# Optimization experiments

Measured on AMD Instinct MI355X. Metric: run time of the kernel, lower is better.

## Reference

```python
import jax, jax.numpy as jnp
import numpy as np

N, D, C = 4096, 2048, 128
MARGIN = 0.3


def _choice(key, mask):
    # Uniform random choice among True entries of mask (Gumbel-max trick).
    g = jax.random.gumbel(key, mask.shape, jnp.float32)
    return jnp.argmax(jnp.where(mask, g, -jnp.inf))


def setup_inputs() -> dict:
    key = jax.random.key(0)
    k1, k2, k3, k4, k5 = jax.random.split(key, 5)
    return {
        "inputs": jax.random.normal(k1, (N, D), jnp.float32),
        "prediction": jax.random.normal(k2, (N, C), jnp.float32),
        "targets": jax.random.randint(k3, (N,), 0, C),
        "true_targets": jax.random.randint(k4, (N,), 0, C),
        "prob": jax.random.uniform(k5, (N,), jnp.float32),
        "threshold": jnp.float32(0.5),
    }


def _forward(inputs, prediction, prob, threshold, targets, true_targets):
    n = inputs.shape[0]
    # Pairwise Euclidean distances: ||xi||^2 + ||xj||^2 - 2 xi.xj  (clamped, sqrt)
    sq = jnp.sum(inputs * inputs, axis=1)
    dist = jnp.sqrt(jnp.clip(sq[:, None] + sq[None, :] - 2.0 * (inputs @ inputs.T), 1e-12, None))
    is_pos = targets[:, None] == targets[None, :]
    confident = prob >= threshold
    pred_cls = jnp.argmax(prediction, axis=1)

    # 12 closest negatives per row (rank 0 = hardest; ranks 1..11 cover the
    # original's fallback loop of at most 10 extra steps, j in 1..11).
    neg_dist = jnp.where(is_pos, jnp.inf, dist)
    _, neg_rank = jax.lax.top_k(-neg_dist, 12)  # [n, 12] indices

    row_keys = jax.random.split(jax.random.key(42), n)
    idx = jnp.arange(n)

    def per_row(i, rk):
        di = dist[i]
        pos_mask = is_pos[i]
        kp, kr = jax.random.split(rk)
        rp = _choice(kp, pos_mask & (idx != i))  # random positive != anchor
        hn = neg_rank[i, 0]                      # hardest negative
        ap0, an0 = di[rp], di[hn]
        p_pos = prob[rp] >= threshold
        p_neg = prob[hn] >= threshold
        is_FN = pred_cls[hn] == targets[i]

        # Case B (pos confident, neg unconfident, false-negative):
        # first confident negative among ranks 1..11, else rank 11.
        cand = neg_rank[i, 1:12]
        conf_c = prob[cand] >= threshold
        hn_new = cand[jnp.where(jnp.any(conf_c), jnp.argmax(conf_c), 10)]
        apB, anB = (ap0 + an0) * 0.5, di[hn_new]

        # Cases C / D-not-FN: resample positive, up to 6 draws total,
        # first draw that is confident and != anchor, else the last draw.
        draws = jax.vmap(lambda k: _choice(k, pos_mask))(jax.random.split(kr, 6))
        valid = (draws != i) & (prob[draws] >= threshold)
        rp_new = draws[jnp.where(jnp.any(valid), jnp.argmax(valid), 5)]
        apC, anC = di[rp_new], (ap0 + an0) * 0.5

        useB = p_pos & ~p_neg & is_FN
        useC = (~p_pos & p_neg) | (~p_pos & ~p_neg & ~is_FN)
        inverse = ~p_pos & ~p_neg & is_FN  # keep ap0/an0, flip hinge direction

        ap = jnp.where(useB, apB, jnp.where(useC, apC, ap0))
        an = jnp.where(useB, anB, jnp.where(useC, anC, an0))
        per_loss = jnp.where(inverse,
                             jnp.maximum(an - ap + MARGIN, 0.0),
                             jnp.maximum(ap - an + MARGIN, 0.0))
        return ap, an, per_loss

    aps, ans, losses = jax.vmap(per_row)(idx, row_keys)
    cnt = jnp.sum(confident)
    loss_sum = jnp.sum(jnp.where(confident, losses, 0.0))
    loss = jnp.where(cnt > 0, loss_sum / jnp.maximum(cnt, 1).astype(loss_sum.dtype),
                     jnp.zeros((), loss_sum.dtype))
    correct = jnp.sum(confident & (ans >= aps))
    return loss, correct, cnt


def reference(inputs, prediction, targets, true_targets, prob, threshold):
    return _forward(inputs, prediction, prob, threshold, targets, true_targets)
```

## Files before the change

kernel.cpp:

```cpp
#include <hip/hip_runtime.h>
#include <hip/hip_bf16.h>
#include <cstdint>
#include <cmath>

#define NROWS 4096
#define DIM   2048
#define CNUM  128
#define MARGIN_F 0.3f
#define TOPK 12
#define MAXM 256
#define GBK 32
#define CAP 160

#define BM 64
#define BN 64
#define BK 16
#define SLICES 8
#define COLS_PER_SLICE (NROWS / SLICES)

typedef _Float16 f16x8 __attribute__((ext_vector_type(8)));
typedef float    f32x4 __attribute__((ext_vector_type(4)));

#define GLD_LDS16(g, l)                                                        \
    __builtin_amdgcn_global_load_lds(                                          \
        (const __attribute__((address_space(1))) uint32_t*)(g),                \
        (__attribute__((address_space(3))) uint32_t*)(l), 16, 0, 0)

__device__ __forceinline__ uint32_t rnd_u32(uint32_t row, uint32_t k) {
    uint64_t x = ((uint64_t)row << 32) ^ (0x9E3779B97F4A7C15ULL * (uint64_t)(k + 1u));
    x ^= x >> 33; x *= 0xff51afd7ed558ccdULL;
    x ^= x >> 33; x *= 0xc4ceb9fe1a85ec53ULL;
    x ^= x >> 33;
    return (uint32_t)x;
}

__global__ void rowsq_kernel(const float* __restrict__ X, float* __restrict__ sq) {
    int wave = (blockIdx.x * blockDim.x + threadIdx.x) >> 6;
    int lane = threadIdx.x & 63;
    if (wave >= NROWS) return;
    const float4* xp = (const float4*)(X + (size_t)wave * DIM);
    float s = 0.f;
    for (int k = lane; k < DIM / 4; k += 64) {
        float4 v = xp[k];
        s += v.x * v.x + v.y * v.y + v.z * v.z + v.w * v.w;
    }
    for (int off = 32; off; off >>= 1) s += __shfl_xor(s, off, 64);
    if (lane == 0) sq[wave] = s;
}

__global__ void predcls_kernel(const float* __restrict__ P, int* __restrict__ cls) {
    int row = (blockIdx.x * blockDim.x + threadIdx.x) >> 6;
    int lane = threadIdx.x & 63;
    if (row >= NROWS) return;
    const float* p = P + (size_t)row * CNUM;
    float v0 = p[lane]; int i0 = lane;
    float v1 = p[lane + 64];
    if (v1 > v0) { v0 = v1; i0 = lane + 64; }
    for (int off = 1; off < 64; off <<= 1) {
        float ov = __shfl_xor(v0, off, 64);
        int   oi = __shfl_xor(i0, off, 64);
        if (ov > v0 || (ov == v0 && oi < i0)) { v0 = ov; i0 = oi; }
    }
    if (lane == 0) cls[row] = i0;
}

__global__ void classlist_kernel(const int* __restrict__ tgt,
                                 int* __restrict__ cnt, int* __restrict__ members) {
    int c = (blockIdx.x * blockDim.x + threadIdx.x) >> 6;
    int lane = threadIdx.x & 63;
    if (c >= CNUM) return;
    int k = 0;
    for (int base = 0; base < NROWS; base += 64) {
        int i = base + lane;
        bool m = (tgt[i] == c);
        unsigned long long mask = __ballot(m);
        if (m) {
            int pos = k + __popcll(mask & ((1ull << lane) - 1ull));
            if (pos < MAXM) members[c * MAXM + pos] = i;
        }
        k += __popcll(mask);
    }
    if (lane == 0) cnt[c] = (k < MAXM) ? k : MAXM;
}

__global__ void convert_kernel(const float* __restrict__ X, _Float16* __restrict__ Xh) {
    int idx = blockIdx.x * blockDim.x + threadIdx.x;
    float4 v = ((const float4*)X)[idx];
    _Float16 h[4] = { (_Float16)v.x, (_Float16)v.y, (_Float16)v.z, (_Float16)v.w };
    ((uint2*)Xh)[idx] = *(uint2*)h;
}

__launch_bounds__(256)
__global__ void mfma_dist_kernel(const _Float16* __restrict__ Xh,
                                 const float* __restrict__ sq, const int* __restrict__ tgt,
                                 float* __restrict__ dist) {
    __shared__ _Float16 Ah[128 * GBK];
    __shared__ _Float16 Bh[128 * GBK];
    __shared__ float    trb[4][16 * 17];
    __shared__ float    sqA[128], sqB[128];
    __shared__ int      tgA[128], tgB[128];

    int b = blockIdx.x;
    int br = 0, S = 0;
    while (b >= S + (32 - br)) { S += 32 - br; br++; }
    int bc = br + (b - S);

    int r0 = br * 128, c0 = bc * 128;
    int tid = threadIdx.x;
    int wave = tid >> 6, lane = tid & 63;
    int wr = wave >> 1, wc = wave & 1;

    if (tid < 128) { sqA[tid] = sq[r0 + tid]; tgA[tid] = tgt[r0 + tid]; }
    else { int t = tid - 128; sqB[t] = sq[c0 + t]; tgB[t] = tgt[c0 + t]; }

    f32x4 acc[4][4];
#pragma unroll
    for (int i = 0; i < 4; i++)
#pragma unroll
        for (int j = 0; j < 4; j++) acc[i][j] = (f32x4)0.f;

    int sr = lane >> 2;
    int sc = (lane & 3) * 8;
    const _Float16* gA0 = Xh + (size_t)(r0 + wave * 16 + sr) * DIM + sc;
    const _Float16* gA1 = Xh + (size_t)(r0 + (wave + 4) * 16 + sr) * DIM + sc;
    const _Float16* gB0 = Xh + (size_t)(c0 + wave * 16 + sr) * DIM + sc;
    const _Float16* gB1 = Xh + (size_t)(c0 + (wave + 4) * 16 + sr) * DIM + sc;
    _Float16* lA0 = &Ah[(wave)     * 16 * GBK];
    _Float16* lA1 = &Ah[(wave + 4) * 16 * GBK];
    _Float16* lB0 = &Bh[(wave)     * 16 * GBK];
    _Float16* lB1 = &Bh[(wave + 4) * 16 * GBK];

    int fr = lane & 15, fq = lane >> 4;
    const int fk = fq * 8;

    for (int kb = 0; kb < DIM; kb += GBK) {
        __syncthreads();
        GLD_LDS16(gA0 + kb, lA0);
        GLD_LDS16(gA1 + kb, lA1);
        GLD_LDS16(gB0 + kb, lB0);
        GLD_LDS16(gB1 + kb, lB1);
        __syncthreads();

        f16x8 af[4], bfr[4];
#pragma unroll
        for (int i = 0; i < 4; i++)
            af[i] = *(const f16x8*)&Ah[(wr * 64 + i * 16 + fr) * GBK + fk];
#pragma unroll
        for (int j = 0; j < 4; j++)
            bfr[j] = *(const f16x8*)&Bh[(wc * 64 + j * 16 + fr) * GBK + fk];
#pragma unroll
        for (int i = 0; i < 4; i++)
#pragma unroll
            for (int j = 0; j < 4; j++)
                acc[i][j] = __builtin_amdgcn_mfma_f32_16x16x32_f16(af[i], bfr[j], acc[i][j], 0, 0, 0);
    }

    float* tb = trb[wave];
#pragma unroll
    for (int i = 0; i < 4; i++) {
#pragma unroll
        for (int j = 0; j < 4; j++) {
            int lcol = wc * 64 + j * 16 + fr;
            float d[4];
#pragma unroll
            for (int r = 0; r < 4; r++) {
                int lrow = wr * 64 + i * 16 + fq * 4 + r;
                float v = sqA[lrow] + sqB[lcol] - 2.f * acc[i][j][r];
                if (tgA[lrow] == tgB[lcol]) v = INFINITY;
                d[r] = v;
                dist[(size_t)(r0 + lrow) * NROWS + (c0 + lcol)] = v;
            }
            if (br != bc) {
#pragma unroll
                for (int r = 0; r < 4; r++) tb[fr * 17 + fq * 4 + r] = d[r];
#pragma unroll
                for (int r = 0; r < 4; r++) {
                    float v = tb[(fq * 4 + r) * 17 + fr];
                    int grow = c0 + wc * 64 + j * 16 + fq * 4 + r;
                    int gcol = r0 + wr * 64 + i * 16 + fr;
                    dist[(size_t)grow * NROWS + gcol] = v;
                }
            }
        }
    }
}

__launch_bounds__(256)
__global__ void topk_kernel(const float* __restrict__ dist,
                            float* __restrict__ top_v, int* __restrict__ top_i) {
    __shared__ float cbv[4][CAP];
    __shared__ int   cbi[4][CAP];
    int wave = threadIdx.x >> 6, lane = threadIdx.x & 63;
    int row = blockIdx.x * 4 + wave;
    const float4* d = (const float4*)(dist + (size_t)row * NROWS);

    float4 v[16];
#pragma unroll
    for (int t = 0; t < 16; t++) v[t] = d[t * 64 + lane];

    float lmin = INFINITY, lmax = -INFINITY, lsum = 0.f;
    int lcnt = 0;
#pragma unroll
    for (int t = 0; t < 16; t++) {
        float xs[4] = { v[t].x, v[t].y, v[t].z, v[t].w };
#pragma unroll
        for (int c = 0; c < 4; c++) {
            float x = xs[c];
            bool fin = x < INFINITY;
            lmin = fminf(lmin, x);
            lmax = fmaxf(lmax, fin ? x : -INFINITY);
            lsum += fin ? x : 0.f;
            lcnt += fin ? 1 : 0;
        }
    }
    for (int off = 32; off; off >>= 1) {
        lmin = fminf(lmin, __shfl_xor(lmin, off, 64));
        lmax = fmaxf(lmax, __shfl_xor(lmax, off, 64));
        lsum += __shfl_xor(lsum, off, 64);
        lcnt += __shfl_xor(lcnt, off, 64);
    }
    float mu = lsum / (float)(lcnt > 0 ? lcnt : 1);

    float lo = lmin, hi = lmax + 1.0f;
    float tau = lmin + 0.3f * (mu - lmin);
    if (!(tau > lo && tau < hi)) tau = 0.5f * (lo + hi);
    for (int it = 0; it < 32; it++) {
        int lc = 0;
#pragma unroll
        for (int t = 0; t < 16; t++) {
            lc += (v[t].x < tau) + (v[t].y < tau) + (v[t].z < tau) + (v[t].w < tau);
        }
        for (int off = 32; off; off >>= 1) lc += __shfl_xor(lc, off, 64);
        if (lc >= TOPK && lc <= CAP) break;
        if (lc < TOPK) lo = tau; else hi = tau;
        tau = 0.5f * (lo + hi);
    }

    int cnt = 0;
#pragma unroll
    for (int t = 0; t < 16; t++) {
        float xs[4] = { v[t].x, v[t].y, v[t].z, v[t].w };
#pragma unroll
        for (int c = 0; c < 4; c++) {
            float x = xs[c];
            bool p = x < tau;
            unsigned long long mk = __ballot(p);
            if (p) {
                int pos = cnt + __popcll(mk & ((1ull << lane) - 1ull));
                if (pos < CAP) {
                    cbv[wave][pos] = x;
                    cbi[wave][pos] = (t * 64 + lane) * 4 + c;
                }
            }
            cnt += __popcll(mk);
        }
    }
    if (cnt > CAP) cnt = CAP;

    float mv[3]; int mi[3];
#pragma unroll
    for (int r = 0; r < 3; r++) {
        int p = r * 64 + lane;
        bool ok = p < cnt;
        mv[r] = ok ? cbv[wave][p] : INFINITY;
        mi[r] = ok ? cbi[wave][p] : 0x7FFFFFFF;
    }

    for (int t = 0; t < TOPK; t++) {
        float bv = mv[0]; int bi = mi[0];
        if (mv[1] < bv || (mv[1] == bv && mi[1] < bi)) { bv = mv[1]; bi = mi[1]; }
        if (mv[2] < bv || (mv[2] == bv && mi[2] < bi)) { bv = mv[2]; bi = mi[2]; }
        for (int off = 32; off; off >>= 1) {
            float ov = __shfl_xor(bv, off, 64);
            int   oi = __shfl_xor(bi, off, 64);
            if (ov < bv || (ov == bv && oi < bi)) { bv = ov; bi = oi; }
        }
        if (lane == 0) {
            top_v[(size_t)row * TOPK + t] = bv;
            int si = (bi >= 0 && bi < NROWS) ? bi : 0;
            top_i[(size_t)row * TOPK + t] = si;
        }
#pragma unroll
        for (int r = 0; r < 3; r++)
            if (mi[r] == bi) { mv[r] = INFINITY; mi[r] = 0x7FFFFFFF; }
    }
}

__launch_bounds__(256)
__global__ void dist_topk_kernel(const float* __restrict__ X, const float* __restrict__ sq,
                                 const int* __restrict__ tgt,
                                 float* __restrict__ part_v, int* __restrict__ part_i) {
    __shared__ float As[BK][BM];
    __shared__ float Bs[BK][BN];
    __shared__ float Cs[BM][BN + 1];
    __shared__ float sqA[BM], sqB[BN];
    __shared__ int   tgA[BM], tgB[BN];

    int rowBase = blockIdx.x * BM;
    int slice = blockIdx.y;
    int tid = threadIdx.x;
    int tx = tid & 15, ty = tid >> 4;

    if (tid < BM) { sqA[tid] = sq[rowBase + tid]; tgA[tid] = tgt[rowBase + tid]; }

    float lv[TOPK]; int li[TOPK];
#pragma unroll
    for (int k = 0; k < TOPK; k++) { lv[k] = INFINITY; li[k] = -1; }

    for (int jt = 0; jt < COLS_PER_SLICE / BN; jt++) {
        int colBase = slice * COLS_PER_SLICE + jt * BN;
        __syncthreads();
        if (tid < BN) { sqB[tid] = sq[colBase + tid]; tgB[tid] = tgt[colBase + tid]; }

        float acc[4][4] = {};
        for (int kb = 0; kb < DIM; kb += BK) {
            int r  = tid >> 2;
            int kk = (tid & 3) * 4;
            float4 va = *(const float4*)(X + (size_t)(rowBase + r) * DIM + kb + kk);
            As[kk + 0][r] = va.x; As[kk + 1][r] = va.y; As[kk + 2][r] = va.z; As[kk + 3][r] = va.w;
            float4 vb = *(const float4*)(X + (size_t)(colBase + r) * DIM + kb + kk);
            Bs[kk + 0][r] = vb.x; Bs[kk + 1][r] = vb.y; Bs[kk + 2][r] = vb.z; Bs[kk + 3][r] = vb.w;
            __syncthreads();
#pragma unroll
            for (int k = 0; k < BK; k++) {
                float a[4], b[4];
                *(float4*)a = *(const float4*)&As[k][ty * 4];
                *(float4*)b = *(const float4*)&Bs[k][tx * 4];
#pragma unroll
                for (int i2 = 0; i2 < 4; i2++)
#pragma unroll
                    for (int j2 = 0; j2 < 4; j2++)
                        acc[i2][j2] += a[i2] * b[j2];
            }
            __syncthreads();
        }
#pragma unroll
        for (int i2 = 0; i2 < 4; i2++) {
            int r = ty * 4 + i2;
#pragma unroll
            for (int j2 = 0; j2 < 4; j2++) {
                int c = tx * 4 + j2;
                float d2 = sqA[r] + sqB[c] - 2.f * acc[i2][j2];
                if (tgA[r] == tgB[c]) d2 = INFINITY;
                Cs[r][c] = d2;
            }
        }
        __syncthreads();
        if (tid < BM) {
            int r = tid;
            for (int c = 0; c < BN; c++) {
                float v = Cs[r][c];
                if (v < lv[TOPK - 1]) {
                    float nv = v; int ni = colBase + c;
#pragma unroll
                    for (int p = 0; p < TOPK; p++) {
                        if (nv < lv[p]) {
                            float tv = lv[p]; int ti = li[p];
                            lv[p] = nv; li[p] = ni;
                            nv = tv; ni = ti;
                        }
                    }
                }
            }
        }
    }
    if (tid < BM) {
        int r = tid;
#pragma unroll
        for (int k = 0; k < TOPK; k++) {
            size_t o = ((size_t)(rowBase + r) * SLICES + slice) * TOPK + k;
            part_v[o] = lv[k];
            part_i[o] = li[k];
        }
    }
}

__global__ void topk_merge_kernel(const float* __restrict__ part_v, const int* __restrict__ part_i,
                                  float* __restrict__ top_v, int* __restrict__ top_i) {
    int row = blockIdx.x * blockDim.x + threadIdx.x;
    if (row >= NROWS) return;
    float lv[TOPK]; int li[TOPK];
#pragma unroll
    for (int k = 0; k < TOPK; k++) { lv[k] = INFINITY; li[k] = -1; }
    for (int s = 0; s < SLICES; s++) {
        for (int k = 0; k < TOPK; k++) {
            size_t o = ((size_t)row * SLICES + s) * TOPK + k;
            float v = part_v[o];
            if (!(v < lv[TOPK - 1])) break;
            int idx = part_i[o];
            float nv = v; int ni = idx;
#pragma unroll
            for (int p = 0; p < TOPK; p++) {
                if (nv < lv[p]) {
                    float tv = lv[p]; int ti = li[p];
                    lv[p] = nv; li[p] = ni;
                    nv = tv; ni = ti;
                }
            }
        }
    }
#pragma unroll
    for (int k = 0; k < TOPK; k++) {
        top_v[(size_t)row * TOPK + k] = lv[k];
        top_i[(size_t)row * TOPK + k] = li[k];
    }
}

__global__ void rowlogic_kernel(const float* __restrict__ X, const float* __restrict__ sq,
                                const float* __restrict__ prob, const float* __restrict__ thr_p,
                                const int* __restrict__ tgt, const int* __restrict__ pred_cls,
                                const int* __restrict__ class_cnt, const int* __restrict__ class_mem,
                                const float* __restrict__ top_v, const int* __restrict__ top_i,
                                float* __restrict__ row_loss, int* __restrict__ row_corr) {
    int i = (blockIdx.x * blockDim.x + threadIdx.x) >> 6;
    int lane = threadIdx.x & 63;
    if (i >= NROWS) return;
    float thr = *thr_p;

    int c = tgt[i];
    int cc = class_cnt[c];
    const int* mem = class_mem + c * MAXM;

    int pos_i = 0;
    for (int k = 0; k < cc; k++) { if (mem[k] == i) { pos_i = k; break; } }

    int rp = 0;
    if (cc > 1) {
        uint32_t r = rnd_u32((uint32_t)i, 0x9111u) % (uint32_t)(cc - 1);
        if ((int)r >= pos_i) r++;
        rp = mem[r];
    }

    int hn = top_i[(size_t)i * TOPK + 0];
    float an0 = sqrtf(fmaxf(top_v[(size_t)i * TOPK + 0], 1e-12f));
    bool p_neg = prob[hn] >= thr;
    bool is_FN = (pred_cls[hn] == c);

    int sel = 11;
    for (int k = 1; k <= 11; k++) {
        int cd = top_i[(size_t)i * TOPK + k];
        if (prob[cd] >= thr) { sel = k; break; }
    }
    float anB = sqrtf(fmaxf(top_v[(size_t)i * TOPK + sel], 1e-12f));

    int first_valid = -1, last_draw = 0;
    for (int k = 0; k < 6; k++) {
        uint32_t r = rnd_u32((uint32_t)i, 0xD000u + (uint32_t)k) % (uint32_t)(cc > 0 ? cc : 1);
        int dk = mem[r];
        last_draw = dk;
        if (first_valid < 0 && dk != i && prob[dk] >= thr) first_valid = dk;
    }
    int rp_new = (first_valid >= 0) ? first_valid : last_draw;
    bool p_pos = prob[rp] >= thr;

    const float4* xi = (const float4*)(X + (size_t)i * DIM);
    const float4* xr = (const float4*)(X + (size_t)rp * DIM);
    const float4* xn = (const float4*)(X + (size_t)rp_new * DIM);
    float s1 = 0.f, s2 = 0.f;
    for (int k = lane; k < DIM / 4; k += 64) {
        float4 a = xi[k], b = xr[k], d = xn[k];
        s1 += a.x * b.x + a.y * b.y + a.z * b.z + a.w * b.w;
        s2 += a.x * d.x + a.y * d.y + a.z * d.z + a.w * d.w;
    }
    for (int off = 32; off; off >>= 1) {
        s1 += __shfl_xor(s1, off, 64);
        s2 += __shfl_xor(s2, off, 64);
    }
    if (lane == 0) {
        float ap0 = sqrtf(fmaxf(sq[i] + sq[rp]     - 2.f * s1, 1e-12f));
        float apC = sqrtf(fmaxf(sq[i] + sq[rp_new] - 2.f * s2, 1e-12f));
        float apB = (ap0 + an0) * 0.5f;
        float anC = (ap0 + an0) * 0.5f;
        bool useB = p_pos && !p_neg && is_FN;
        bool useC = (!p_pos && p_neg) || (!p_pos && !p_neg && !is_FN);
        bool inverse = !p_pos && !p_neg && is_FN;
        float ap = useB ? apB : (useC ? apC : ap0);
        float an = useB ? anB : (useC ? anC : an0);
        float pl = inverse ? fmaxf(an - ap + MARGIN_F, 0.f)
                           : fmaxf(ap - an + MARGIN_F, 0.f);
        bool conf = prob[i] >= thr;
        row_loss[i] = conf ? pl : 0.f;
        row_corr[i] = (conf && (an >= ap)) ? 1 : 0;
    }
}

__global__ void reduce_kernel(const float* __restrict__ row_loss, const int* __restrict__ row_corr,
                              const float* __restrict__ prob, const float* __restrict__ thr_p,
                              float* __restrict__ out) {
    __shared__ float sl[256];
    __shared__ int   sc[256];
    __shared__ int   sn[256];
    float thr = *thr_p;
    int tid = threadIdx.x;
    float l = 0.f; int corr = 0, cnt = 0;
    for (int i = tid; i < NROWS; i += 256) {
        l += row_loss[i];
        corr += row_corr[i];
        cnt += (prob[i] >= thr) ? 1 : 0;
    }
    sl[tid] = l; sc[tid] = corr; sn[tid] = cnt;
    __syncthreads();
    for (int off = 128; off; off >>= 1) {
        if (tid < off) {
            sl[tid] += sl[tid + off];
            sc[tid] += sc[tid + off];
            sn[tid] += sn[tid + off];
        }
        __syncthreads();
    }
    if (tid == 0) {
        int cn = sn[0];
        float loss = (cn > 0) ? (sl[0] / (float)(cn > 1 ? cn : 1)) : 0.f;
        out[0] = loss;
        out[1] = (float)sc[0];
        out[2] = (float)cn;
    }
}

extern "C" void kernel_launch(void* const* d_in, const int* in_sizes, int n_in,
                              void* d_out, int out_size, void* d_ws, size_t ws_size,
                              hipStream_t stream) {
    const float* X    = (const float*)d_in[0];
    const float* P    = (const float*)d_in[1];
    const int*   tgt  = (const int*)d_in[2];
    const float* prob = (const float*)d_in[4];
    const float* thr  = (const float*)d_in[5];
    float* out = (float*)d_out;

    char* w = (char*)d_ws;
    auto alloc = [&](size_t bytes) {
        char* p = w;
        w += (bytes + 255) & ~(size_t)255;
        return p;
    };
    float* sq        = (float*)alloc(NROWS * sizeof(float));
    int*   pred_cls  = (int*)  alloc(NROWS * sizeof(int));
    int*   class_cnt = (int*)  alloc(CNUM * sizeof(int));
    int*   class_mem = (int*)  alloc((size_t)CNUM * MAXM * sizeof(int));
    float* top_v     = (float*)alloc((size_t)NROWS * TOPK * sizeof(float));
    int*   top_i     = (int*)  alloc((size_t)NROWS * TOPK * sizeof(int));
    float* row_loss  = (float*)alloc(NROWS * sizeof(float));
    int*   row_corr  = (int*)  alloc(NROWS * sizeof(int));
    char*  var_base  = w;

    size_t fast_need = (size_t)NROWS * DIM * 2 + (size_t)NROWS * NROWS * 4 + (1 << 20);
    bool fast = ((size_t)(var_base - (char*)d_ws) + fast_need) <= ws_size;

    rowsq_kernel<<<NROWS / 4, 256, 0, stream>>>(X, sq);
    predcls_kernel<<<NROWS / 4, 256, 0, stream>>>(P, pred_cls);
    classlist_kernel<<<CNUM / 4, 256, 0, stream>>>(tgt, class_cnt, class_mem);

    if (fast) {
        _Float16* Xh   = (_Float16*)alloc((size_t)NROWS * DIM * 2);
        float*    dist = (float*)alloc((size_t)NROWS * NROWS * 4);
        convert_kernel<<<(NROWS * DIM / 4) / 256, 256, 0, stream>>>(X, Xh);
        mfma_dist_kernel<<<528, 256, 0, stream>>>(Xh, sq, tgt, dist);
        topk_kernel<<<NROWS / 4, 256, 0, stream>>>(dist, top_v, top_i);
    } else {
        float* part_v = (float*)alloc((size_t)NROWS * SLICES * TOPK * sizeof(float));
        int*   part_i = (int*)  alloc((size_t)NROWS * SLICES * TOPK * sizeof(int));
        dist_topk_kernel<<<dim3(NROWS / BM, SLICES), 256, 0, stream>>>(X, sq, tgt, part_v, part_i);
        topk_merge_kernel<<<NROWS / 256, 256, 0, stream>>>(part_v, part_i, top_v, top_i);
    }

    rowlogic_kernel<<<NROWS / 4, 256, 0, stream>>>(X, sq, prob, thr, tgt, pred_cls,
                                                   class_cnt, class_mem, top_v, top_i,
                                                   row_loss, row_corr);
    reduce_kernel<<<1, 256, 0, stream>>>(row_loss, row_corr, prob, thr, out);
}
```

Baseline: 258.1 us.

## Double-buffer MFMA distance GEMM with swizzled LDS and fuse row norms into conversion

The fp16 pairwise-distance GEMM now uses double-buffered LDS tiles with a 64-wide K step and an XOR swizzle. The next tile's global-to-LDS load is issued before computing the current one, so memory latency overlaps MFMA work and LDS bank conflicts drop. Row squared norms are computed inside the fp32-to-fp16 conversion kernel, removing a separate pass over X. LDS use doubles and launch bounds request two blocks per CU, which may pressure registers.

```diff
diff --git a/kernel.cpp b/kernel.cpp
--- a/kernel.cpp
+++ b/kernel.cpp
@@ -9,7 +9,7 @@
 #define MARGIN_F 0.3f
 #define TOPK 12
 #define MAXM 256
-#define GBK 32
+#define GBK2 64
 #define CAP 160
 
 #define BM 64
@@ -46,6 +46,24 @@
     }
     for (int off = 32; off; off >>= 1) s += __shfl_xor(s, off, 64);
     if (lane == 0) sq[wave] = s;
+}
+
+__global__ void prep_kernel(const float* __restrict__ X, _Float16* __restrict__ Xh,
+                            float* __restrict__ sq) {
+    __shared__ float ws[4];
+    int row = blockIdx.x, tid = threadIdx.x;
+    int wave = tid >> 6, lane = tid & 63;
+    const float4* xp = (const float4*)(X + (size_t)row * DIM);
+    float4 a = xp[tid * 2], b = xp[tid * 2 + 1];
+    float s = a.x * a.x + a.y * a.y + a.z * a.z + a.w * a.w
+            + b.x * b.x + b.y * b.y + b.z * b.z + b.w * b.w;
+    _Float16 h[8] = { (_Float16)a.x, (_Float16)a.y, (_Float16)a.z, (_Float16)a.w,
+                      (_Float16)b.x, (_Float16)b.y, (_Float16)b.z, (_Float16)b.w };
+    ((uint4*)(Xh + (size_t)row * DIM))[tid] = *(uint4*)h;
+    for (int off = 32; off; off >>= 1) s += __shfl_xor(s, off, 64);
+    if (lane == 0) ws[wave] = s;
+    __syncthreads();
+    if (tid == 0) sq[row] = ws[0] + ws[1] + ws[2] + ws[3];
 }
 
 __global__ void predcls_kernel(const float* __restrict__ P, int* __restrict__ cls) {
@@ -83,19 +101,12 @@
     if (lane == 0) cnt[c] = (k < MAXM) ? k : MAXM;
 }
 
-__global__ void convert_kernel(const float* __restrict__ X, _Float16* __restrict__ Xh) {
-    int idx = blockIdx.x * blockDim.x + threadIdx.x;
-    float4 v = ((const float4*)X)[idx];
-    _Float16 h[4] = { (_Float16)v.x, (_Float16)v.y, (_Float16)v.z, (_Float16)v.w };
-    ((uint2*)Xh)[idx] = *(uint2*)h;
-}
-
-__launch_bounds__(256)
+__launch_bounds__(256, 2)
 __global__ void mfma_dist_kernel(const _Float16* __restrict__ Xh,
                                  const float* __restrict__ sq, const int* __restrict__ tgt,
                                  float* __restrict__ dist) {
-    __shared__ _Float16 Ah[128 * GBK];
-    __shared__ _Float16 Bh[128 * GBK];
+    __shared__ _Float16 Ah[2][128 * GBK2];
+    __shared__ _Float16 Bh[2][128 * GBK2];
     __shared__ float    trb[4][16 * 17];
     __shared__ float    sqA[128], sqB[128];
     __shared__ int      tgA[128], tgB[128];
@@ -119,40 +130,53 @@
 #pragma unroll
         for (int j = 0; j < 4; j++) acc[i][j] = (f32x4)0.f;
 
-    int sr = lane >> 2;
-    int sc = (lane & 3) * 8;
-    const _Float16* gA0 = Xh + (size_t)(r0 + wave * 16 + sr) * DIM + sc;
-    const _Float16* gA1 = Xh + (size_t)(r0 + (wave + 4) * 16 + sr) * DIM + sc;
-    const _Float16* gB0 = Xh + (size_t)(c0 + wave * 16 + sr) * DIM + sc;
-    const _Float16* gB1 = Xh + (size_t)(c0 + (wave + 4) * 16 + sr) * DIM + sc;
-    _Float16* lA0 = &Ah[(wave)     * 16 * GBK];
-    _Float16* lA1 = &Ah[(wave + 4) * 16 * GBK];
-    _Float16* lB0 = &Bh[(wave)     * 16 * GBK];
-    _Float16* lB1 = &Bh[(wave + 4) * 16 * GBK];
-
+    const _Float16* gA[4]; const _Float16* gB[4];
+    int ldsOff[4];
+#pragma unroll
+    for (int q = 0; q < 4; q++) {
+        int r = wave * 32 + q * 8 + (lane >> 3);
+        int j = (lane & 7) ^ (r & 7);
+        gA[q] = Xh + (size_t)(r0 + r) * DIM + j * 8;
+        gB[q] = Xh + (size_t)(c0 + r) * DIM + j * 8;
+        ldsOff[q] = (wave * 32 + q * 8) * GBK2;
+    }
+
+    auto stage = [&](int buf, int kOff) {
+#pragma unroll
+        for (int q = 0; q < 4; q++) {
+            GLD_LDS16(gA[q] + kOff, &Ah[buf][ldsOff[q]]);
+            GLD_LDS16(gB[q] + kOff, &Bh[buf][ldsOff[q]]);
+        }
+    };
+
+    stage(0, 0);
     int fr = lane & 15, fq = lane >> 4;
-    const int fk = fq * 8;
-
-    for (int kb = 0; kb < DIM; kb += GBK) {
+
+    for (int it = 0; it < DIM / GBK2; it++) {
+        int cur = it & 1;
         __syncthreads();
-        GLD_LDS16(gA0 + kb, lA0);
-        GLD_LDS16(gA1 + kb, lA1);
-        GLD_LDS16(gB0 + kb, lB0);
-        GLD_LDS16(gB1 + kb, lB1);
-        __syncthreads();
-
-        f16x8 af[4], bfr[4];
-#pragma unroll
-        for (int i = 0; i < 4; i++)
-            af[i] = *(const f16x8*)&Ah[(wr * 64 + i * 16 + fr) * GBK + fk];
-#pragma unroll
-        for (int j = 0; j < 4; j++)
-            bfr[j] = *(const f16x8*)&Bh[(wc * 64 + j * 16 + fr) * GBK + fk];
-#pragma unroll
-        for (int i = 0; i < 4; i++)
-#pragma unroll
-            for (int j = 0; j < 4; j++)
-                acc[i][j] = __builtin_amdgcn_mfma_f32_16x16x32_f16(af[i], bfr[j], acc[i][j], 0, 0, 0);
+        if (it + 1 < DIM / GBK2) stage(cur ^ 1, (it + 1) * GBK2);
+#pragma unroll
+        for (int s = 0; s < 2; s++) {
+            f16x8 af[4], bf[4];
+#pragma unroll
+            for (int i = 0; i < 4; i++) {
+                int row = wr * 64 + i * 16 + fr;
+                int jj = (s * 4 + fq) ^ (row & 7);
+                af[i] = *(const f16x8*)&Ah[cur][row * GBK2 + jj * 8];
+            }
+#pragma unroll
+            for (int j = 0; j < 4; j++) {
+                int col = wc * 64 + j * 16 + fr;
+                int jj = (s * 4 + fq) ^ (col & 7);
+                bf[j] = *(const f16x8*)&Bh[cur][col * GBK2 + jj * 8];
+            }
+#pragma unroll
+            for (int i = 0; i < 4; i++)
+#pragma unroll
+                for (int j = 0; j < 4; j++)
+                    acc[i][j] = __builtin_amdgcn_mfma_f32_16x16x32_f16(af[i], bf[j], acc[i][j], 0, 0, 0);
+        }
     }
 
     float* tb = trb[wave];
@@ -546,17 +570,17 @@
     size_t fast_need = (size_t)NROWS * DIM * 2 + (size_t)NROWS * NROWS * 4 + (1 << 20);
     bool fast = ((size_t)(var_base - (char*)d_ws) + fast_need) <= ws_size;
 
-    rowsq_kernel<<<NROWS / 4, 256, 0, stream>>>(X, sq);
     predcls_kernel<<<NROWS / 4, 256, 0, stream>>>(P, pred_cls);
     classlist_kernel<<<CNUM / 4, 256, 0, stream>>>(tgt, class_cnt, class_mem);
 
     if (fast) {
         _Float16* Xh   = (_Float16*)alloc((size_t)NROWS * DIM * 2);
         float*    dist = (float*)alloc((size_t)NROWS * NROWS * 4);
-        convert_kernel<<<(NROWS * DIM / 4) / 256, 256, 0, stream>>>(X, Xh);
+        prep_kernel<<<NROWS, 256, 0, stream>>>(X, Xh, sq);
         mfma_dist_kernel<<<528, 256, 0, stream>>>(Xh, sq, tgt, dist);
         topk_kernel<<<NROWS / 4, 256, 0, stream>>>(dist, top_v, top_i);
     } else {
+        rowsq_kernel<<<NROWS / 4, 256, 0, stream>>>(X, sq);
         float* part_v = (float*)alloc((size_t)NROWS * SLICES * TOPK * sizeof(float));
         int*   part_i = (int*)  alloc((size_t)NROWS * SLICES * TOPK * sizeof(int));
         dist_topk_kernel<<<dim3(NROWS / BM, SLICES), 256, 0, stream>>>(X, sq, tgt, part_v, part_i);
```

Result: faster. 235.8 us (-8.6%).
